# Optimization experiments

Hardware: AMD Instinct MI355X
Metric: run time of the kernel (lower is better)

The kernel has to match this reference:

```python
import jax, jax.numpy as jnp
import numpy as np

B, D_IN, HID, DIM, M = 4096, 128, 200, 256, 32
SIGMA, OMEGA = 1.0, 1.7
LB, UB = 0.0, 1.0


def setup_inputs() -> dict:
    key = jax.random.key(0)
    ks = jax.random.split(key, 9)
    s = lambda d: 1.0 / jnp.sqrt(jnp.float32(d))
    return {
        "x": jax.random.normal(ks[0], (B, D_IN), jnp.float32),
        "b": jax.random.uniform(ks[1], (B, M), jnp.float32),
        "W1": jax.random.normal(ks[2], (D_IN, HID), jnp.float32) * s(D_IN),
        "b1": jnp.zeros((HID,), jnp.float32),
        "W2": jax.random.normal(ks[3], (HID, HID), jnp.float32) * s(HID),
        "b2": jnp.zeros((HID,), jnp.float32),
        "W3": jax.random.normal(ks[4], (HID, DIM), jnp.float32) * s(HID),
        "b3": jnp.zeros((DIM,), jnp.float32),
        "A": jax.random.normal(ks[5], (M, DIM), jnp.float32) * s(DIM),
        "step": 1000,
        "n_iter": 100,
    }


def reference(x, b, W1, b1, W2, b2, W3, b3, A, step, n_iter):
    # --- MLP: Dense(200) -> relu -> Dense(200) -> relu -> Dense(dim) ---
    h = jax.nn.relu(x @ W1 + b1)
    h = jax.nn.relu(h @ W2 + b2)
    y = h @ W3 + b3  # [B, DIM]

    # schedule = linear_schedule(0.0, 0.0, ...) -> alpha == 0.0 always
    alpha = jnp.float32(0.0)

    # --- projection onto {z : A z = b, LB <= z <= UB} via relaxed
    # Douglas-Rachford / SOR fixed-point iteration (sigma/omega) ---
    AAt_inv = jnp.linalg.inv(A @ A.T + 1e-6 * jnp.eye(M, dtype=A.dtype))

    def p_aff(z):  # affine equality projection, z: [B, DIM]
        r = z @ A.T - b            # [B, M] residual
        return z - (r @ AAt_inv) @ A

    def p_box(z):
        return jnp.clip(z, LB, UB)

    def body(z, _):
        u = p_aff(z)
        v = p_box(2.0 * u - z)     # reflection then box projection
        z = z + SIGMA * OMEGA * (v - u)
        return z, None

    z0 = y  # project.get_init(x): initialize fixed point at MLP output
    z_final, _ = jax.lax.scan(body, z0, None, length=n_iter)
    proj = p_aff(z_final)

    # interpolation between raw MLP output and projection (alpha == 0)
    out = alpha * y + (1.0 - alpha) * proj
    return out
```

## Files before the change

### kernel.cpp

```cpp
#include <hip/hip_runtime.h>
#include <hip/hip_bf16.h>

typedef float    f4v    __attribute__((ext_vector_type(4)));
typedef short    short8 __attribute__((ext_vector_type(8)));
typedef unsigned u2v    __attribute__((ext_vector_type(2)));

constexpr int Bn = 4096, TR = 16;

__device__ inline unsigned cvt2(float x, float y) {
  union { __hip_bfloat162 h; unsigned u; } c;
  c.h = __float22bfloat162_rn(float2{x, y});
  return c.u;
}
__device__ inline void split_pair(float x, float y, unsigned& hp, unsigned& lp) {
  hp = cvt2(x, y);
  float hx = __uint_as_float(hp << 16);
  float hy = __uint_as_float(hp & 0xffff0000u);
  lp = cvt2(x - hx, y - hy);
}
union S8U { unsigned u[4]; short8 s; };
__device__ inline void split8(const float v[8], short8& hi, short8& lo) {
  S8U h, l;
  #pragma unroll
  for (int d = 0; d < 4; ++d) split_pair(v[2 * d], v[2 * d + 1], h.u[d], l.u[d]);
  hi = h.s; lo = l.s;
}
__device__ inline void split8p(const float* p, short8& hi, short8& lo) {
  f4v a = *(const f4v*)p, b = *(const f4v*)(p + 4);
  float v[8] = {a[0], a[1], a[2], a[3], b[0], b[1], b[2], b[3]};
  split8(v, hi, lo);
}
__device__ inline f4v mfma16(short8 a, short8 b, f4v c) {
  return __builtin_amdgcn_mfma_f32_16x16x32_bf16(a, b, c, 0, 0, 0);
}
__device__ __attribute__((always_inline)) inline f4v gdot8(
    const short8 (&ah)[8], const short8 (&al)[8],
    const short8 (&bh)[8], const short8 (&bl)[8]) {
  f4v c = {0.f, 0.f, 0.f, 0.f};
  #pragma unroll
  for (int s = 0; s < 8; ++s) {
    c = mfma16(ah[s], bh[s], c);
    c = mfma16(al[s], bh[s], c);
    c = mfma16(ah[s], bl[s], c);
  }
  return c;
}

__device__ inline void pack_write(unsigned* dst, float z0, float z1, float z2, float z3) {
  unsigned a0, b0, a1, b1;
  split_pair(z0, z1, a0, b0);
  split_pair(z2, z3, a1, b1);
  u2v hv; hv[0] = a0; hv[1] = a1;
  u2v lv; lv[0] = b0; lv[1] = b1;
  *(u2v*)&dst[0]   = hv;
  *(u2v*)&dst[256] = lv;
}

__global__ __launch_bounds__(256) void k_prep(const float* __restrict__ A,
                                              float* __restrict__ KAT) {
  __shared__ __align__(16) float As[32 * 256];
  __shared__ float Gm[32 * 68];
  __shared__ float GinvL[32 * 32];

  const int t = threadIdx.x;
  const int lane = t & 63, wv = t >> 6, quad = lane >> 4, l15 = lane & 15;
  const int T = wv & 1, kh = wv >> 1;

  for (int i = t; i < 2048; i += 256)
    ((f4v*)As)[i] = ((const f4v*)A)[i];
  __syncthreads();

  {
    short8 afh[2][8], afl[2][8];
    #pragma unroll
    for (int tt = 0; tt < 2; ++tt)
      #pragma unroll
      for (int s = 0; s < 8; ++s)
        split8p(As + (l15 + 16 * tt) * 256 + 32 * s + 8 * quad,
                afh[tt][s], afl[tt][s]);
    f4v cg;
    if      (wv == 0) cg = gdot8(afh[0], afl[0], afh[0], afl[0]);
    else if (wv == 1) cg = gdot8(afh[1], afl[1], afh[0], afl[0]);
    else if (wv == 2) cg = gdot8(afh[0], afl[0], afh[1], afl[1]);
    else              cg = gdot8(afh[1], afl[1], afh[1], afl[1]);
    #pragma unroll
    for (int r = 0; r < 4; ++r) {
      int gi = 16 * T + 4 * quad + r, gj = 16 * kh + l15;
      Gm[gi * 68 + gj]      = cg[r] + (gi == gj ? 1e-6f : 0.f);
      Gm[gi * 68 + 32 + gj] = (gi == gj) ? 1.f : 0.f;
    }
  }
  __syncthreads();

  if (wv == 0) {
    float gcol[32];
    #pragma unroll
    for (int i = 0; i < 32; ++i) gcol[i] = Gm[i * 68 + lane];
    #pragma unroll
    for (int k = 0; k < 32; ++k) {
      float ckk  = __shfl(gcol[k], k);
      float ipiv = 1.f / ckk;
      float pivj = gcol[k] * ipiv;
      gcol[k] = pivj;
      #pragma unroll
      for (int i = 0; i < 32; ++i) {
        if (i == k) continue;
        float cki = __shfl(gcol[i], k);
        gcol[i] = fmaf(-cki, pivj, gcol[i]);
      }
    }
    if (lane >= 32) {
      #pragma unroll
      for (int i = 0; i < 32; ++i) GinvL[i * 32 + (lane - 32)] = gcol[i];
    }
  }
  __syncthreads();

  {
    float res[32];
    #pragma unroll
    for (int m = 0; m < 32; ++m) res[m] = 0.f;
    for (int p = 0; p < 32; ++p) {
      float av = As[p * 256 + t];
      #pragma unroll
      for (int m4 = 0; m4 < 8; ++m4) {
        f4v g = *(const f4v*)&GinvL[p * 32 + 4 * m4];
        res[4 * m4 + 0] = fmaf(av, g[0], res[4 * m4 + 0]);
        res[4 * m4 + 1] = fmaf(av, g[1], res[4 * m4 + 1]);
        res[4 * m4 + 2] = fmaf(av, g[2], res[4 * m4 + 2]);
        res[4 * m4 + 3] = fmaf(av, g[3], res[4 * m4 + 3]);
      }
    }
    #pragma unroll
    for (int m4 = 0; m4 < 8; ++m4) {
      f4v v = {res[4 * m4], res[4 * m4 + 1], res[4 * m4 + 2], res[4 * m4 + 3]};
      *(f4v*)&KAT[t * 32 + 4 * m4] = v;
    }
  }
}

__global__ __launch_bounds__(256) void k_prep2(const float* __restrict__ A,
                                               const float* __restrict__ KAT,
                                               unsigned* __restrict__ QTH,
                                               unsigned* __restrict__ QTL) {
  const int t = threadIdx.x, lane = t & 63, wv = t >> 6;
  const int n = blockIdx.x * 4 + wv;
  const int k0 = lane * 4;
  const float* kr = KAT + n * 32;
  f4v p = {0.f, 0.f, 0.f, 0.f};
  #pragma unroll
  for (int m = 0; m < 32; ++m) {
    float km = kr[m];
    f4v av = *(const f4v*)&A[m * 256 + k0];
    p[0] = fmaf(km, av[0], p[0]);
    p[1] = fmaf(km, av[1], p[1]);
    p[2] = fmaf(km, av[2], p[2]);
    p[3] = fmaf(km, av[3], p[3]);
  }
  float q0 = ((k0 + 0) == n ? 1.f : 0.f) - p[0];
  float q1 = ((k0 + 1) == n ? 1.f : 0.f) - p[1];
  float q2 = ((k0 + 2) == n ? 1.f : 0.f) - p[2];
  float q3 = ((k0 + 3) == n ? 1.f : 0.f) - p[3];
  unsigned a0, b0, a1, b1;
  split_pair(q0, q1, a0, b0);
  split_pair(q2, q3, a1, b1);
  u2v hv; hv[0] = a0; hv[1] = a1;
  u2v lv; lv[0] = b0; lv[1] = b1;
  *(u2v*)&QTH[n * 128 + lane * 2] = hv;
  *(u2v*)&QTL[n * 128 + lane * 2] = lv;
}

__global__ __launch_bounds__(512, 2) void k_main(
    const float* __restrict__ x,  const float* __restrict__ bmat,
    const float* __restrict__ W1, const float* __restrict__ b1,
    const float* __restrict__ W2, const float* __restrict__ b2,
    const float* __restrict__ W3, const float* __restrict__ b3,
    const float* __restrict__ KAT,
    const short* __restrict__ QTHs, const short* __restrict__ QTLs,
    const int* __restrict__ n_iter_p, float* __restrict__ out) {

  __shared__ __align__(16) float    ubuf[8768];
  __shared__ __align__(16) unsigned zfrag[8192];

  const int t = threadIdx.x;
  const int lane = t & 63, wv = t >> 6, quad = lane >> 4, l15 = lane & 15;
  const int row0 = blockIdx.x * TR;

  float* xs = ubuf;
  float* h1 = ubuf + 2112;
  float* h2 = ubuf + 5440;
  float* ys = ubuf;

  if (t < 512) {
    int r = t >> 5, c4 = t & 31;
    *(f4v*)&xs[r * 132 + 4 * c4] = *(const f4v*)&x[(size_t)(row0 + r) * 128 + 4 * c4];
  }
  __syncthreads();

  {
    const int rg = wv, oc = lane;
    const bool g3 = (oc < 8);
    float acc[4][2];

    #pragma unroll
    for (int oi = 0; oi < 4; ++oi) { acc[oi][0] = 0.f; acc[oi][1] = 0.f; }
    for (int k4 = 0; k4 < 32; ++k4) {
      f4v xv0 = *(const f4v*)&xs[(2 * rg + 0) * 132 + 4 * k4];
      f4v xv1 = *(const f4v*)&xs[(2 * rg + 1) * 132 + 4 * k4];
      #pragma unroll
      for (int kk = 0; kk < 4; ++kk) {
        const float* wr = W1 + (4 * k4 + kk) * 200 + oc;
        float w0 = wr[0], w1c = wr[64], w2c = wr[128];
        float w3c = g3 ? wr[192] : 0.f;
        acc[0][0] = fmaf(xv0[kk], w0, acc[0][0]);  acc[0][1] = fmaf(xv1[kk], w0, acc[0][1]);
        acc[1][0] = fmaf(xv0[kk], w1c, acc[1][0]); acc[1][1] = fmaf(xv1[kk], w1c, acc[1][1]);
        acc[2][0] = fmaf(xv0[kk], w2c, acc[2][0]); acc[2][1] = fmaf(xv1[kk], w2c, acc[2][1]);
        acc[3][0] = fmaf(xv0[kk], w3c, acc[3][0]); acc[3][1] = fmaf(xv1[kk], w3c, acc[3][1]);
      }
    }
    #pragma unroll
    for (int oi = 0; oi < 4; ++oi) {
      if (oi == 3 && !g3) continue;
      float bb = b1[oc + 64 * oi];
      h1[(2 * rg + 0) * 208 + oc + 64 * oi] = fmaxf(acc[oi][0] + bb, 0.f);
      h1[(2 * rg + 1) * 208 + oc + 64 * oi] = fmaxf(acc[oi][1] + bb, 0.f);
    }
    __syncthreads();

    #pragma unroll
    for (int oi = 0; oi < 4; ++oi) { acc[oi][0] = 0.f; acc[oi][1] = 0.f; }
    for (int k4 = 0; k4 < 50; ++k4) {
      f4v xv0 = *(const f4v*)&h1[(2 * rg + 0) * 208 + 4 * k4];
      f4v xv1 = *(const f4v*)&h1[(2 * rg + 1) * 208 + 4 * k4];
      #pragma unroll
      for (int kk = 0; kk < 4; ++kk) {
        const float* wr = W2 + (4 * k4 + kk) * 200 + oc;
        float w0 = wr[0], w1c = wr[64], w2c = wr[128];
        float w3c = g3 ? wr[192] : 0.f;
        acc[0][0] = fmaf(xv0[kk], w0, acc[0][0]);  acc[0][1] = fmaf(xv1[kk], w0, acc[0][1]);
        acc[1][0] = fmaf(xv0[kk], w1c, acc[1][0]); acc[1][1] = fmaf(xv1[kk], w1c, acc[1][1]);
        acc[2][0] = fmaf(xv0[kk], w2c, acc[2][0]); acc[2][1] = fmaf(xv1[kk], w2c, acc[2][1]);
        acc[3][0] = fmaf(xv0[kk], w3c, acc[3][0]); acc[3][1] = fmaf(xv1[kk], w3c, acc[3][1]);
      }
    }
    #pragma unroll
    for (int oi = 0; oi < 4; ++oi) {
      if (oi == 3 && !g3) continue;
      float bb = b2[oc + 64 * oi];
      h2[(2 * rg + 0) * 208 + oc + 64 * oi] = fmaxf(acc[oi][0] + bb, 0.f);
      h2[(2 * rg + 1) * 208 + oc + 64 * oi] = fmaxf(acc[oi][1] + bb, 0.f);
    }
    __syncthreads();

    #pragma unroll
    for (int oi = 0; oi < 4; ++oi) { acc[oi][0] = 0.f; acc[oi][1] = 0.f; }
    for (int k4 = 0; k4 < 50; ++k4) {
      f4v xv0 = *(const f4v*)&h2[(2 * rg + 0) * 208 + 4 * k4];
      f4v xv1 = *(const f4v*)&h2[(2 * rg + 1) * 208 + 4 * k4];
      #pragma unroll
      for (int kk = 0; kk < 4; ++kk) {
        const float* wr = W3 + (4 * k4 + kk) * 256 + oc;
        float w0 = wr[0], w1c = wr[64], w2c = wr[128], w3c = wr[192];
        acc[0][0] = fmaf(xv0[kk], w0, acc[0][0]);  acc[0][1] = fmaf(xv1[kk], w0, acc[0][1]);
        acc[1][0] = fmaf(xv0[kk], w1c, acc[1][0]); acc[1][1] = fmaf(xv1[kk], w1c, acc[1][1]);
        acc[2][0] = fmaf(xv0[kk], w2c, acc[2][0]); acc[2][1] = fmaf(xv1[kk], w2c, acc[2][1]);
        acc[3][0] = fmaf(xv0[kk], w3c, acc[3][0]); acc[3][1] = fmaf(xv1[kk], w3c, acc[3][1]);
      }
    }
    __syncthreads();
    #pragma unroll
    for (int oi = 0; oi < 4; ++oi) {
      float bb = b3[oc + 64 * oi];
      ys[(2 * rg + 0) * 260 + oc + 64 * oi] = acc[oi][0] + bb;
      ys[(2 * rg + 1) * 260 + oc + 64 * oi] = acc[oi][1] + bb;
    }
  }
  __syncthreads();

  short8 qh[2][8], ql[2][8];
  #pragma unroll
  for (int u = 0; u < 2; ++u) {
    const int n = 16 * (2 * wv + u) + l15;
    #pragma unroll
    for (int s = 0; s < 8; ++s) {
      qh[u][s] = *(const short8*)&QTHs[n * 256 + 32 * s + 8 * quad];
      ql[u][s] = *(const short8*)&QTLs[n * 256 + 32 * s + 8 * quad];
    }
  }

  float bv[32];
  #pragma unroll
  for (int m4 = 0; m4 < 8; ++m4)
    *(f4v*)&bv[4 * m4] = *(const f4v*)&bmat[(size_t)(row0 + l15) * 32 + 4 * m4];
  f4v crv[2];
  #pragma unroll
  for (int u = 0; u < 2; ++u) {
    #pragma unroll
    for (int r = 0; r < 4; ++r) {
      const float* kp = KAT + (size_t)(16 * (2 * wv + u) + 4 * quad + r) * 32;
      float s = 0.f;
      #pragma unroll
      for (int m4 = 0; m4 < 8; ++m4) {
        f4v kv = *(const f4v*)&kp[4 * m4];
        s = fmaf(bv[4 * m4 + 0], kv[0], s);
        s = fmaf(bv[4 * m4 + 1], kv[1], s);
        s = fmaf(bv[4 * m4 + 2], kv[2], s);
        s = fmaf(bv[4 * m4 + 3], kv[3], s);
      }
      crv[u][r] = s;
    }
  }

  int zoff[2];
  float zr[2][4];
  #pragma unroll
  for (int u = 0; u < 2; ++u) {
    const int U = 2 * wv + u;
    const int qp = 2 * (U & 1) + (quad >> 1);
    zoff[u] = ((U >> 1) * 2) * 256 + qp * 64 + l15 * 4 + 2 * (quad & 1);
    f4v yv = *(const f4v*)&ys[l15 * 260 + 16 * U + 4 * quad];
    #pragma unroll
    for (int r = 0; r < 4; ++r) zr[u][r] = yv[r];
    pack_write(&zfrag[zoff[u]], zr[u][0], zr[u][1], zr[u][2], zr[u][3]);
  }
  __syncthreads();

  const int niter = n_iter_p[0];
  const int zrd = lane * 4;

  for (int it = 0; it <= niter; ++it) {
    const unsigned* zb = zfrag + ((it & 1) << 12);
    unsigned*       zw = zfrag + (((it & 1) ^ 1) << 12);

    f4v uA[2], uB[2], uC[2];
    #pragma unroll
    for (int u = 0; u < 2; ++u) {
      uA[u] = crv[u];
      uB[u] = (f4v){0.f, 0.f, 0.f, 0.f};
      uC[u] = (f4v){0.f, 0.f, 0.f, 0.f};
    }
    #pragma unroll
    for (int s = 0; s < 8; ++s) {
      short8 zh = *(const short8*)&zb[(2 * s + 0) * 256 + zrd];
      short8 zl = *(const short8*)&zb[(2 * s + 1) * 256 + zrd];
      #pragma unroll
      for (int u = 0; u < 2; ++u) uA[u] = mfma16(qh[u][s], zh, uA[u]);
      #pragma unroll
      for (int u = 0; u < 2; ++u) uB[u] = mfma16(ql[u][s], zh, uB[u]);
      #pragma unroll
      for (int u = 0; u < 2; ++u) uC[u] = mfma16(qh[u][s], zl, uC[u]);
    }

    if (it < niter) {
      #pragma unroll
      for (int u = 0; u < 2; ++u) {
        float zn[4];
        #pragma unroll
        for (int r = 0; r < 4; ++r) {
          float uv = (uA[u][r] + uB[u][r]) + uC[u][r];
          float z  = zr[u][r];
          float vv = fminf(fmaxf(fmaf(2.f, uv, -z), 0.f), 1.f);
          zn[r] = fmaf(1.7f, vv - uv, z);
          zr[u][r] = zn[r];
        }
        pack_write(&zw[zoff[u]], zn[0], zn[1], zn[2], zn[3]);
      }
      __syncthreads();
    } else {
      #pragma unroll
      for (int u = 0; u < 2; ++u) {
        const int U = 2 * wv + u;
        f4v ov;
        #pragma unroll
        for (int r = 0; r < 4; ++r) ov[r] = (uA[u][r] + uB[u][r]) + uC[u][r];
        *(f4v*)&out[(size_t)(row0 + l15) * 256 + 16 * U + 4 * quad] = ov;
      }
    }
  }
}

extern "C" void kernel_launch(void* const* d_in, const int* in_sizes, int n_in,
                              void* d_out, int out_size, void* d_ws, size_t ws_size,
                              hipStream_t stream) {
  const float* x    = (const float*)d_in[0];
  const float* bmat = (const float*)d_in[1];
  const float* W1   = (const float*)d_in[2];
  const float* b1   = (const float*)d_in[3];
  const float* W2   = (const float*)d_in[4];
  const float* b2   = (const float*)d_in[5];
  const float* W3   = (const float*)d_in[6];
  const float* b3   = (const float*)d_in[7];
  const float* A    = (const float*)d_in[8];
  const int*  n_it  = (const int*)d_in[10];

  float*    KAT = (float*)d_ws;
  unsigned* QTH = (unsigned*)((char*)d_ws + 32768);
  unsigned* QTL = QTH + 256 * 128;
  float* out = (float*)d_out;

  hipLaunchKernelGGL(k_prep,  dim3(1),       dim3(256), 0, stream, A, KAT);
  hipLaunchKernelGGL(k_prep2, dim3(64),      dim3(256), 0, stream, A, KAT, QTH, QTL);
  hipLaunchKernelGGL(k_main,  dim3(Bn / TR), dim3(512), 0, stream,
                     x, bmat, W1, b1, W2, b2, W3, b3, KAT,
                     (const short*)QTH, (const short*)QTL, n_it, out);
}
```

Before: 262.1 us.

## Double block to 1024 threads and split the fixed-point K dimension across wave pairs

```diff
diff --git a/kernel.cpp b/kernel.cpp
--- a/kernel.cpp
+++ b/kernel.cpp
@@ -170,7 +170,8 @@
   *(u2v*)&QTL[n * 128 + lane * 2] = lv;
 }
 
-__global__ __launch_bounds__(512, 2) void k_main(
+__global__ __launch_bounds__(1024, 4)
+void k_main(
     const float* __restrict__ x,  const float* __restrict__ bmat,
     const float* __restrict__ W1, const float* __restrict__ b1,
     const float* __restrict__ W2, const float* __restrict__ b2,
@@ -180,7 +181,7 @@
     const int* __restrict__ n_iter_p, float* __restrict__ out) {
 
   __shared__ __align__(16) float    ubuf[8768];
-  __shared__ __align__(16) unsigned zfrag[8192];
+  __shared__ __align__(16) unsigned zfrag[12288];
 
   const int t = threadIdx.x;
   const int lane = t & 63, wv = t >> 6, quad = lane >> 4, l15 = lane & 15;
@@ -198,106 +199,89 @@
   __syncthreads();
 
   {
-    const int rg = wv, oc = lane;
+    const int rr = wv, oc = lane;
     const bool g3 = (oc < 8);
-    float acc[4][2];
-
-    #pragma unroll
-    for (int oi = 0; oi < 4; ++oi) { acc[oi][0] = 0.f; acc[oi][1] = 0.f; }
+    float acc[4];
+
+    #pragma unroll
+    for (int oi = 0; oi < 4; ++oi) acc[oi] = 0.f;
     for (int k4 = 0; k4 < 32; ++k4) {
-      f4v xv0 = *(const f4v*)&xs[(2 * rg + 0) * 132 + 4 * k4];
-      f4v xv1 = *(const f4v*)&xs[(2 * rg + 1) * 132 + 4 * k4];
+      f4v xv = *(const f4v*)&xs[rr * 132 + 4 * k4];
       #pragma unroll
       for (int kk = 0; kk < 4; ++kk) {
         const float* wr = W1 + (4 * k4 + kk) * 200 + oc;
         float w0 = wr[0], w1c = wr[64], w2c = wr[128];
         float w3c = g3 ? wr[192] : 0.f;
-        acc[0][0] = fmaf(xv0[kk], w0, acc[0][0]);  acc[0][1] = fmaf(xv1[kk], w0, acc[0][1]);
-        acc[1][0] = fmaf(xv0[kk], w1c, acc[1][0]); acc[1][1] = fmaf(xv1[kk], w1c, acc[1][1]);
-        acc[2][0] = fmaf(xv0[kk], w2c, acc[2][0]); acc[2][1] = fmaf(xv1[kk], w2c, acc[2][1]);
-        acc[3][0] = fmaf(xv0[kk], w3c, acc[3][0]); acc[3][1] = fmaf(xv1[kk], w3c, acc[3][1]);
+        acc[0] = fmaf(xv[kk], w0, acc[0]);
+        acc[1] = fmaf(xv[kk], w1c, acc[1]);
+        acc[2] = fmaf(xv[kk], w2c, acc[2]);
+        acc[3] = fmaf(xv[kk], w3c, acc[3]);
       }
     }
     #pragma unroll
     for (int oi = 0; oi < 4; ++oi) {
       if (oi == 3 && !g3) continue;
-      float bb = b1[oc + 64 * oi];
-      h1[(2 * rg + 0) * 208 + oc + 64 * oi] = fmaxf(acc[oi][0] + bb, 0.f);
-      h1[(2 * rg + 1) * 208 + oc + 64 * oi] = fmaxf(acc[oi][1] + bb, 0.f);
-    }
-    __syncthreads();
-
-    #pragma unroll
-    for (int oi = 0; oi < 4; ++oi) { acc[oi][0] = 0.f; acc[oi][1] = 0.f; }
+      h1[rr * 208 + oc + 64 * oi] = fmaxf(acc[oi] + b1[oc + 64 * oi], 0.f);
+    }
+    __syncthreads();
+
+    #pragma unroll
+    for (int oi = 0; oi < 4; ++oi) acc[oi] = 0.f;
     for (int k4 = 0; k4 < 50; ++k4) {
-      f4v xv0 = *(const f4v*)&h1[(2 * rg + 0) * 208 + 4 * k4];
-      f4v xv1 = *(const f4v*)&h1[(2 * rg + 1) * 208 + 4 * k4];
+      f4v xv = *(const f4v*)&h1[rr * 208 + 4 * k4];
       #pragma unroll
       for (int kk = 0; kk < 4; ++kk) {
         const float* wr = W2 + (4 * k4 + kk) * 200 + oc;
         float w0 = wr[0], w1c = wr[64], w2c = wr[128];
         float w3c = g3 ? wr[192] : 0.f;
-        acc[0][0] = fmaf(xv0[kk], w0, acc[0][0]);  acc[0][1] = fmaf(xv1[kk], w0, acc[0][1]);
-        acc[1][0] = fmaf(xv0[kk], w1c, acc[1][0]); acc[1][1] = fmaf(xv1[kk], w1c, acc[1][1]);
-        acc[2][0] = fmaf(xv0[kk], w2c, acc[2][0]); acc[2][1] = fmaf(xv1[kk], w2c, acc[2][1]);
-        acc[3][0] = fmaf(xv0[kk], w3c, acc[3][0]); acc[3][1] = fmaf(xv1[kk], w3c, acc[3][1]);
-      }
-    }
+        acc[0] = fmaf(xv[kk], w0, acc[0]);
+        acc[1] = fmaf(xv[kk], w1c, acc[1]);
+        acc[2] = fmaf(xv[kk], w2c, acc[2]);
+        acc[3] = fmaf(xv[kk], w3c, acc[3]);
+      }
+    }
+    __syncthreads();
     #pragma unroll
     for (int oi = 0; oi < 4; ++oi) {
       if (oi == 3 && !g3) continue;
-      float bb = b2[oc + 64 * oi];
-      h2[(2 * rg + 0) * 208 + oc + 64 * oi] = fmaxf(acc[oi][0] + bb, 0.f);
-      h2[(2 * rg + 1) * 208 + oc + 64 * oi] = fmaxf(acc[oi][1] + bb, 0.f);
-    }
-    __syncthreads();
-
-    #pragma unroll
-    for (int oi = 0; oi < 4; ++oi) { acc[oi][0] = 0.f; acc[oi][1] = 0.f; }
+      h2[rr * 208 + oc + 64 * oi] = fmaxf(acc[oi] + b2[oc + 64 * oi], 0.f);
+    }
+    __syncthreads();
+
+    #pragma unroll
+    for (int oi = 0; oi < 4; ++oi) acc[oi] = 0.f;
     for (int k4 = 0; k4 < 50; ++k4) {
-      f4v xv0 = *(const f4v*)&h2[(2 * rg + 0) * 208 + 4 * k4];
-      f4v xv1 = *(const f4v*)&h2[(2 * rg + 1) * 208 + 4 * k4];
+      f4v xv = *(const f4v*)&h2[rr * 208 + 4 * k4];
       #pragma unroll
       for (int kk = 0; kk < 4; ++kk) {
         const float* wr = W3 + (4 * k4 + kk) * 256 + oc;
         float w0 = wr[0], w1c = wr[64], w2c = wr[128], w3c = wr[192];
-        acc[0][0] = fmaf(xv0[kk], w0, acc[0][0]);  acc[0][1] = fmaf(xv1[kk], w0, acc[0][1]);
-        acc[1][0] = fmaf(xv0[kk], w1c, acc[1][0]); acc[1][1] = fmaf(xv1[kk], w1c, acc[1][1]);
-        acc[2][0] = fmaf(xv0[kk], w2c, acc[2][0]); acc[2][1] = fmaf(xv1[kk], w2c, acc[2][1]);
-        acc[3][0] = fmaf(xv0[kk], w3c, acc[3][0]); acc[3][1] = fmaf(xv1[kk], w3c, acc[3][1]);
-      }
-    }
-    __syncthreads();
-    #pragma unroll
-    for (int oi = 0; oi < 4; ++oi) {
-      float bb = b3[oc + 64 * oi];
-      ys[(2 * rg + 0) * 260 + oc + 64 * oi] = acc[oi][0] + bb;
-      ys[(2 * rg + 1) * 260 + oc + 64 * oi] = acc[oi][1] + bb;
-    }
-  }
-  __syncthreads();
-
-  short8 qh[2][8], ql[2][8];
-  #pragma unroll
-  for (int u = 0; u < 2; ++u) {
-    const int n = 16 * (2 * wv + u) + l15;
-    #pragma unroll
-    for (int s = 0; s < 8; ++s) {
-      qh[u][s] = *(const short8*)&QTHs[n * 256 + 32 * s + 8 * quad];
-      ql[u][s] = *(const short8*)&QTLs[n * 256 + 32 * s + 8 * quad];
-    }
-  }
-
-  float bv[32];
-  #pragma unroll
-  for (int m4 = 0; m4 < 8; ++m4)
-    *(f4v*)&bv[4 * m4] = *(const f4v*)&bmat[(size_t)(row0 + l15) * 32 + 4 * m4];
-  f4v crv[2];
-  #pragma unroll
-  for (int u = 0; u < 2; ++u) {
+        acc[0] = fmaf(xv[kk], w0, acc[0]);
+        acc[1] = fmaf(xv[kk], w1c, acc[1]);
+        acc[2] = fmaf(xv[kk], w2c, acc[2]);
+        acc[3] = fmaf(xv[kk], w3c, acc[3]);
+      }
+    }
+    __syncthreads();
+    #pragma unroll
+    for (int oi = 0; oi < 4; ++oi)
+      ys[rr * 260 + oc + 64 * oi] = acc[oi] + b3[oc + 64 * oi];
+  }
+  __syncthreads();
+
+  const int ng = wv & 7, kh = wv >> 3;
+  const int Uown = 2 * ng + kh;
+  const int Upar = 2 * ng + 1 - kh;
+
+  f4v crv;
+  {
+    float bv[32];
+    #pragma unroll
+    for (int m4 = 0; m4 < 8; ++m4)
+      *(f4v*)&bv[4 * m4] = *(const f4v*)&bmat[(size_t)(row0 + l15) * 32 + 4 * m4];
     #pragma unroll
     for (int r = 0; r < 4; ++r) {
-      const float* kp = KAT + (size_t)(16 * (2 * wv + u) + 4 * quad + r) * 32;
+      const float* kp = KAT + (size_t)(16 * Uown + 4 * quad + r) * 32;
       float s = 0.f;
       #pragma unroll
       for (int m4 = 0; m4 < 8; ++m4) {
@@ -307,74 +291,79 @@
         s = fmaf(bv[4 * m4 + 2], kv[2], s);
         s = fmaf(bv[4 * m4 + 3], kv[3], s);
       }
-      crv[u][r] = s;
-    }
-  }
-
-  int zoff[2];
-  float zr[2][4];
-  #pragma unroll
-  for (int u = 0; u < 2; ++u) {
-    const int U = 2 * wv + u;
-    const int qp = 2 * (U & 1) + (quad >> 1);
-    zoff[u] = ((U >> 1) * 2) * 256 + qp * 64 + l15 * 4 + 2 * (quad & 1);
-    f4v yv = *(const f4v*)&ys[l15 * 260 + 16 * U + 4 * quad];
-    #pragma unroll
-    for (int r = 0; r < 4; ++r) zr[u][r] = yv[r];
-    pack_write(&zfrag[zoff[u]], zr[u][0], zr[u][1], zr[u][2], zr[u][3]);
+      crv[r] = s;
+    }
+  }
+  asm volatile("" : "+v"(crv));
+
+  short8 qhO[4], qlO[4], qhP[4], qlP[4];
+  #pragma unroll
+  for (int so = 0; so < 4; ++so) {
+    const int s = 4 * kh + so;
+    const int nO = 16 * Uown + l15, nP = 16 * Upar + l15;
+    qhO[so] = *(const short8*)&QTHs[nO * 256 + 32 * s + 8 * quad];
+    qlO[so] = *(const short8*)&QTLs[nO * 256 + 32 * s + 8 * quad];
+    qhP[so] = *(const short8*)&QTHs[nP * 256 + 32 * s + 8 * quad];
+    qlP[so] = *(const short8*)&QTLs[nP * 256 + 32 * s + 8 * quad];
+  }
+  #pragma unroll
+  for (int so = 0; so < 4; ++so)
+    asm volatile("" : "+v"(qhO[so]), "+v"(qlO[so]), "+v"(qhP[so]), "+v"(qlP[so]));
+
+  const int qp = 2 * (Uown & 1) + (quad >> 1);
+  const int zoff = ((Uown >> 1) * 2) * 256 + qp * 64 + l15 * 4 + 2 * (quad & 1);
+  float zr[4];
+  {
+    f4v yv = *(const f4v*)&ys[l15 * 260 + 16 * Uown + 4 * quad];
+    #pragma unroll
+    for (int r = 0; r < 4; ++r) zr[r] = yv[r];
+    pack_write(&zfrag[zoff], zr[0], zr[1], zr[2], zr[3]);
   }
   __syncthreads();
 
   const int niter = n_iter_p[0];
   const int zrd = lane * 4;
+  float* pbuf = ubuf;
+  const int pwr = (Upar * 64 + lane) * 4;
+  const int prd = (Uown * 64 + lane) * 4;
 
   for (int it = 0; it <= niter; ++it) {
     const unsigned* zb = zfrag + ((it & 1) << 12);
     unsigned*       zw = zfrag + (((it & 1) ^ 1) << 12);
 
-    f4v uA[2], uB[2], uC[2];
-    #pragma unroll
-    for (int u = 0; u < 2; ++u) {
-      uA[u] = crv[u];
-      uB[u] = (f4v){0.f, 0.f, 0.f, 0.f};
-      uC[u] = (f4v){0.f, 0.f, 0.f, 0.f};
-    }
-    #pragma unroll
-    for (int s = 0; s < 8; ++s) {
+    f4v uAo = {0.f,0.f,0.f,0.f}, uBo = {0.f,0.f,0.f,0.f}, uCo = {0.f,0.f,0.f,0.f};
+    f4v uAp = {0.f,0.f,0.f,0.f}, uBp = {0.f,0.f,0.f,0.f}, uCp = {0.f,0.f,0.f,0.f};
+    #pragma unroll
+    for (int so = 0; so < 4; ++so) {
+      const int s = 4 * kh + so;
       short8 zh = *(const short8*)&zb[(2 * s + 0) * 256 + zrd];
       short8 zl = *(const short8*)&zb[(2 * s + 1) * 256 + zrd];
-      #pragma unroll
-      for (int u = 0; u < 2; ++u) uA[u] = mfma16(qh[u][s], zh, uA[u]);
-      #pragma unroll
-      for (int u = 0; u < 2; ++u) uB[u] = mfma16(ql[u][s], zh, uB[u]);
-      #pragma unroll
-      for (int u = 0; u < 2; ++u) uC[u] = mfma16(qh[u][s], zl, uC[u]);
-    }
+      uAo = mfma16(qhO[so], zh, uAo);
+      uAp = mfma16(qhP[so], zh, uAp);
+      uBo = mfma16(qlO[so], zh, uBo);
+      uBp = mfma16(qlP[so], zh, uBp);
+      uCo = mfma16(qhO[so], zl, uCo);
+      uCp = mfma16(qhP[so], zl, uCp);
+    }
+    f4v pO = (uAo + uBo) + uCo;
+    f4v pP = (uAp + uBp) + uCp;
+    *(f4v*)&pbuf[pwr] = pP;
+    __syncthreads();
+    f4v uf = (pO + *(const f4v*)&pbuf[prd]) + crv;
 
     if (it < niter) {
-      #pragma unroll
-      for (int u = 0; u < 2; ++u) {
-        float zn[4];
-        #pragma unroll
-        for (int r = 0; r < 4; ++r) {
-          float uv = (uA[u][r] + uB[u][r]) + uC[u][r];
-          float z  = zr[u][r];
-          float vv = fminf(fmaxf(fmaf(2.f, uv, -z), 0.f), 1.f);
-          zn[r] = fmaf(1.7f, vv - uv, z);
-          zr[u][r] = zn[r];
-        }
-        pack_write(&zw[zoff[u]], zn[0], zn[1], zn[2], zn[3]);
-      }
+      float zn[4];
+      #pragma unroll
+      for (int r = 0; r < 4; ++r) {
+        float uv = uf[r], z = zr[r];
+        float vv = fminf(fmaxf(fmaf(2.f, uv, -z), 0.f), 1.f);
+        zn[r] = fmaf(1.7f, vv - uv, z);
+        zr[r] = zn[r];
+      }
+      pack_write(&zw[zoff], zn[0], zn[1], zn[2], zn[3]);
       __syncthreads();
     } else {
-      #pragma unroll
-      for (int u = 0; u < 2; ++u) {
-        const int U = 2 * wv + u;
-        f4v ov;
-        #pragma unroll
-        for (int r = 0; r < 4; ++r) ov[r] = (uA[u][r] + uB[u][r]) + uC[u][r];
-        *(f4v*)&out[(size_t)(row0 + l15) * 256 + 16 * U + 4 * quad] = ov;
-      }
+      *(f4v*)&out[(size_t)(row0 + l15) * 256 + 16 * Uown + 4 * quad] = uf;
     }
   }
 }
@@ -400,7 +389,7 @@
 
   hipLaunchKernelGGL(k_prep,  dim3(1),       dim3(256), 0, stream, A, KAT);
   hipLaunchKernelGGL(k_prep2, dim3(64),      dim3(256), 0, stream, A, KAT, QTH, QTL);
-  hipLaunchKernelGGL(k_main,  dim3(Bn / TR), dim3(512), 0, stream,
+  hipLaunchKernelGGL(k_main,  dim3(Bn / TR), dim3(1024), 0, stream,
                      x, bmat, W1, b1, W2, b2, W3, b3, KAT,
                      (const short*)QTH, (const short*)QTL, n_it, out);
 }
```

New measurement: 698.0 us. 166% more time.
